# Kernel optimization log

Hardware: AMD Instinct MI355X
Metric: run time of the kernel (lower is better)

Reference implementation:

```python
import jax, jax.numpy as jnp
import numpy as np

B, S, E = 4, 2048, 1024


def setup_inputs() -> dict:
    key = jax.random.key(0)
    k1, k2, k3, k4 = jax.random.split(key, 4)
    scale = 1.0 / np.sqrt(E)
    return {
        "x": jax.random.normal(k1, (B, S, E), dtype=jnp.float32),
        "W_Q": jax.random.normal(k2, (E, E), dtype=jnp.float32) * scale,
        "W_K": jax.random.normal(k3, (E, E), dtype=jnp.float32) * scale,
        "W_V": jax.random.normal(k4, (E, E), dtype=jnp.float32) * scale,
    }


def reference(x, W_Q, W_K, W_V):
    # nn.Linear(E, E, bias=False): y = x @ W.T
    Q = jnp.einsum("bse,fe->bsf", x, W_Q)
    K = jnp.einsum("bse,fe->bsf", x, W_K)
    V = jnp.einsum("bse,fe->bsf", x, W_V)
    d = Q.shape[-1]
    scores = jnp.einsum("bqd,bkd->bqk", Q, K) / jnp.sqrt(jnp.float32(d))
    # causal mask: -inf strictly above the diagonal
    seq = Q.shape[1]
    causal = jnp.tril(jnp.ones((seq, seq), dtype=bool))  # [S,S]
    scores = jnp.where(causal[None, :, :], scores, jnp.float32(-jnp.inf))
    attn = jax.nn.softmax(scores, axis=-1)
    return jnp.einsum("bqk,bkd->bqd", attn, V)
```

## Files before the change

### kernel.cpp

```cpp
#include <hip/hip_runtime.h>
#include <hip/hip_bf16.h>
#include <stdint.h>

typedef __hip_bfloat16 bf16;
typedef __attribute__((ext_vector_type(8))) short bf16x8;
typedef __attribute__((ext_vector_type(4))) float f32x4;
typedef __attribute__((ext_vector_type(8))) unsigned short u16x8;
typedef __attribute__((ext_vector_type(4))) unsigned short u16x4;

#define SLEN 2048
#define ED   1024
#define NB   4
#define AS1 __attribute__((address_space(1)))
#define AS3 __attribute__((address_space(3)))
#define SB0() __builtin_amdgcn_sched_barrier(0)

static __device__ __forceinline__ unsigned short f2bf(float f) {
    return __builtin_bit_cast(unsigned short, __float2bfloat16(f));
}

__device__ __forceinline__ void gemm_core(
    const char* __restrict__ aT, int lda,
    const char* __restrict__ bT, int ldb,
    int nkt, char* sm, int tid, f32x4 (&acc)[4][4])
{
    const int lane = tid & 63, wave = tid >> 6;
    const int wm = wave >> 1, wn = wave & 1;
    const int fr = lane & 15, kc = lane >> 4;

    auto STAGE = [&](int kh, int Tn) {
        char* buf = sm + (Tn & 1) * 49152;
#pragma unroll
        for (int j = 0; j < 2; ++j) {
            int rid = j * 512 + tid;
            int row = rid >> 2, c = rid & 3;
            const char* src = aT + (size_t)row * lda + Tn * 128 + kh * 64
                            + ((c ^ ((row >> 1) & 3)) * 16);
            __builtin_amdgcn_global_load_lds(
                (const AS1 uint32_t*)src,
                (AS3 uint32_t*)(buf + kh * 16384 + (j * 512 + wave * 64) * 16),
                16, 0, 0);
        }
        {
            int row = tid >> 2, c = tid & 3;
            const char* src = bT + (size_t)row * ldb + Tn * 128 + kh * 64
                            + ((c ^ ((row >> 1) & 3)) * 16);
            __builtin_amdgcn_global_load_lds(
                (const AS1 uint32_t*)src,
                (AS3 uint32_t*)(buf + 32768 + kh * 8192 + (wave * 64) * 16),
                16, 0, 0);
        }
    };
    auto RD = [&](int T, int kh, bf16x8 (&a)[4], bf16x8 (&b)[4]) {
        const char* buf = sm + (T & 1) * 49152;
#pragma unroll
        for (int i = 0; i < 4; ++i) {
            int row = wm * 64 + i * 16 + fr;
            a[i] = *(const bf16x8*)(buf + kh * 16384 + row * 64
                                    + ((kc ^ ((row >> 1) & 3)) * 16));
        }
#pragma unroll
        for (int i = 0; i < 4; ++i) {
            int row = wn * 64 + i * 16 + fr;
            b[i] = *(const bf16x8*)(buf + 32768 + kh * 8192 + row * 64
                                    + ((kc ^ ((row >> 1) & 3)) * 16));
        }
    };
    auto MM = [&](bf16x8 (&a)[4], bf16x8 (&b)[4]) {
        __builtin_amdgcn_s_setprio(1);
#pragma unroll
        for (int i = 0; i < 4; ++i)
#pragma unroll
            for (int n = 0; n < 4; ++n)
                acc[i][n] = __builtin_amdgcn_mfma_f32_16x16x32_bf16(
                    a[i], b[n], acc[i][n], 0, 0, 0);
        __builtin_amdgcn_s_setprio(0);
    };

    STAGE(0, 0); STAGE(1, 0);
    asm volatile("s_waitcnt vmcnt(3)" ::: "memory");
    SB0();
    __builtin_amdgcn_s_barrier();

    bf16x8 aE[4], bE[4], aO[4], bO[4];
    for (int T = 0; T < nkt; ++T) {
        const bool pre = (T + 1 < nkt);
        RD(T, 0, aE, bE);
        SB0();
        if (pre) STAGE(0, T + 1);
        SB0();
        if (T > 0) {
            asm volatile("s_waitcnt lgkmcnt(8)" ::: "memory");
            SB0();
            MM(aO, bO);
        }
        if (pre) asm volatile("s_waitcnt vmcnt(3)" ::: "memory");
        else     asm volatile("s_waitcnt vmcnt(0)" ::: "memory");
        SB0();
        __builtin_amdgcn_s_barrier();
        RD(T, 1, aO, bO);
        SB0();
        if (pre) STAGE(1, T + 1);
        SB0();
        asm volatile("s_waitcnt lgkmcnt(8)" ::: "memory");
        SB0();
        MM(aE, bE);
        if (pre) asm volatile("s_waitcnt vmcnt(3)" ::: "memory");
        else     asm volatile("s_waitcnt vmcnt(0)" ::: "memory");
        SB0();
        __builtin_amdgcn_s_barrier();
    }
    asm volatile("s_waitcnt lgkmcnt(0)" ::: "memory");
    SB0();
    MM(aO, bO);
}

__global__ __launch_bounds__(256) void convert_to_bf16(
    const float* __restrict__ x, const float* __restrict__ wq,
    const float* __restrict__ wk, const float* __restrict__ wv,
    bf16* __restrict__ xb, bf16* __restrict__ wqb,
    bf16* __restrict__ wkb, bf16* __restrict__ wvb)
{
    long g = (long)blockIdx.x * 256 + threadIdx.x;
    const float* src; bf16* dst; long o;
    if (g < 1048576) { src = x; dst = xb; o = g * 8; }
    else {
        long g2 = g - 1048576;
        int w = (int)(g2 >> 17);
        o = (g2 & 131071) * 8;
        src = (w == 0) ? wq : (w == 1) ? wk : wv;
        dst = (w == 0) ? wqb : (w == 1) ? wkb : wvb;
    }
    float4 v0 = *(const float4*)(src + o);
    float4 v1 = *(const float4*)(src + o + 4);
    u16x8 r;
    r[0] = f2bf(v0.x); r[1] = f2bf(v0.y); r[2] = f2bf(v0.z); r[3] = f2bf(v0.w);
    r[4] = f2bf(v1.x); r[5] = f2bf(v1.y); r[6] = f2bf(v1.z); r[7] = f2bf(v1.w);
    *(u16x8*)(dst + o) = r;
}

__global__ __launch_bounds__(512, 2) void qkv_gemm(
    const bf16* __restrict__ xb, const bf16* __restrict__ wqb,
    const bf16* __restrict__ wkb, const bf16* __restrict__ wvb,
    bf16* __restrict__ Qb, bf16* __restrict__ Kb, bf16* __restrict__ Vt)
{
    extern __shared__ char smem[];
    int bid = blockIdx.x, tid = threadIdx.x;
    int xcd = bid & 7, i = bid >> 3;
    int tm = (xcd << 2) | (i & 3);
    int tn = i >> 2;
    const bf16* W = (tn < 8) ? wqb : (tn < 16) ? wkb : wvb;
    int tnl = tn & 7;
    f32x4 acc[4][4] = {};
    gemm_core((const char*)(xb + (size_t)tm * 256 * ED), ED * 2,
              (const char*)(W + (size_t)tnl * 128 * ED), ED * 2,
              16, smem, tid, acc);

    int lane = tid & 63, wave = tid >> 6, wm = wave >> 1, wn = wave & 1;
    int rl = (lane >> 4) * 4, cl = lane & 15;
    if (tn < 16) {
        bf16* C = (tn < 8) ? Qb : Kb;
#pragma unroll
        for (int mf = 0; mf < 4; ++mf)
#pragma unroll
            for (int j = 0; j < 4; ++j) {
                int r = tm * 256 + wm * 64 + mf * 16 + rl + j;
#pragma unroll
                for (int nf = 0; nf < 4; ++nf) {
                    int c = tnl * 128 + wn * 64 + nf * 16 + cl;
                    C[(size_t)r * ED + c] = __float2bfloat16(acc[mf][nf][j]);
                }
            }
    } else {
#pragma unroll
        for (int mf = 0; mf < 4; ++mf)
#pragma unroll
            for (int j = 0; j < 4; ++j) {
                int r = tm * 256 + wm * 64 + mf * 16 + rl + j;
                int bb = r >> 11, s = r & 2047;
#pragma unroll
                for (int nf = 0; nf < 4; ++nf) {
                    int d = tnl * 128 + wn * 64 + nf * 16 + cl;
                    Vt[(((size_t)bb << 10) + d) * SLEN + s] = __float2bfloat16(acc[mf][nf][j]);
                }
            }
    }
}

__global__ __launch_bounds__(512, 2) void qk_gemm(
    const bf16* __restrict__ Qb, const bf16* __restrict__ Kb, float* __restrict__ Sc)
{
    extern __shared__ char smem[];
    int bx = blockIdx.x, b = blockIdx.y, tid = threadIdx.x;
    int t = (bx & 7) * 9 + (bx >> 3);
    int ti = 0;
    while ((ti + 1) * (ti + 2) <= t) ++ti;
    int tj = t - ti * (ti + 1);
    f32x4 acc[4][4] = {};
    gemm_core((const char*)(Qb + ((size_t)b * SLEN + ti * 256) * ED), ED * 2,
              (const char*)(Kb + ((size_t)b * SLEN + tj * 128) * ED), ED * 2,
              16, smem, tid, acc);

    float* Sb = Sc + (size_t)b * SLEN * SLEN;
    int lane = tid & 63, wave = tid >> 6, wm = wave >> 1, wn = wave & 1;
    int rl = (lane >> 4) * 4, cl = lane & 15;
#pragma unroll
    for (int mf = 0; mf < 4; ++mf)
#pragma unroll
        for (int j = 0; j < 4; ++j) {
            int r = ti * 256 + wm * 64 + mf * 16 + rl + j;
#pragma unroll
            for (int nf = 0; nf < 4; ++nf) {
                int c = tj * 128 + wn * 64 + nf * 16 + cl;
                Sb[(size_t)r * SLEN + c] = acc[mf][nf][j] * 0.03125f;
            }
        }
}

__global__ __launch_bounds__(256) void softmax_rows(float* __restrict__ Sc)
{
    int q = blockIdx.x, b = blockIdx.y, tid = threadIdx.x;
    float* row = Sc + ((size_t)b * SLEN + q) * SLEN;
    int lane = tid & 63, wave = tid >> 6;
    __shared__ float red[4];

    float vals[8];
    float lmax = -3.0e38f;
#pragma unroll
    for (int r = 0; r < 2; ++r) {
        int i4 = tid + r * 256;
        if (i4 * 4 <= q) {
            float4 v = *(const float4*)(row + i4 * 4);
            vals[r * 4 + 0] = v.x; vals[r * 4 + 1] = v.y;
            vals[r * 4 + 2] = v.z; vals[r * 4 + 3] = v.w;
#pragma unroll
            for (int e = 0; e < 4; ++e) {
                int k = i4 * 4 + e;
                if (k <= q) lmax = fmaxf(lmax, vals[r * 4 + e]);
            }
        }
    }
#pragma unroll
    for (int o = 32; o > 0; o >>= 1) lmax = fmaxf(lmax, __shfl_xor(lmax, o));
    if (lane == 0) red[wave] = lmax;
    __syncthreads();
    float m = fmaxf(fmaxf(red[0], red[1]), fmaxf(red[2], red[3]));
    __syncthreads();
    float lsum = 0.f;
#pragma unroll
    for (int r = 0; r < 2; ++r) {
        int i4 = tid + r * 256;
        if (i4 * 4 <= q)
#pragma unroll
            for (int e = 0; e < 4; ++e) {
                int k = i4 * 4 + e;
                if (k <= q) lsum += __expf(vals[r * 4 + e] - m);
            }
    }
#pragma unroll
    for (int o = 32; o > 0; o >>= 1) lsum += __shfl_xor(lsum, o);
    if (lane == 0) red[wave] = lsum;
    __syncthreads();
    float inv = 1.0f / (red[0] + red[1] + red[2] + red[3]);
    unsigned short* prow = (unsigned short*)row;
#pragma unroll
    for (int r = 0; r < 2; ++r) {
        int i4 = tid + r * 256;
        u16x4 o4;
#pragma unroll
        for (int e = 0; e < 4; ++e) {
            int k = i4 * 4 + e;
            float p = (k <= q) ? __expf(vals[r * 4 + e] - m) * inv : 0.0f;
            o4[e] = f2bf(p);
        }
        *(u16x4*)(prow + i4 * 4) = o4;
    }
}

__global__ __launch_bounds__(512, 2) void pv_gemm(
    const bf16* __restrict__ P, const bf16* __restrict__ Vt, float* __restrict__ O)
{
    extern __shared__ char smem[];
    int mq = 7 - blockIdx.x, nd = blockIdx.y, b = blockIdx.z, tid = threadIdx.x;
    f32x4 acc[4][4] = {};
    int nkt = (mq + 1) * 4;
    gemm_core((const char*)P + ((size_t)b * SLEN + mq * 256) * 8192, 8192,
              (const char*)(Vt + ((size_t)b * ED + nd * 128) * SLEN), SLEN * 2,
              nkt, smem, tid, acc);

    int lane = tid & 63, wave = tid >> 6, wm = wave >> 1, wn = wave & 1;
    int rl = (lane >> 4) * 4, cl = lane & 15;
    float* Ob = O + (size_t)b * SLEN * ED;
#pragma unroll
    for (int mf = 0; mf < 4; ++mf)
#pragma unroll
        for (int j = 0; j < 4; ++j) {
            int r = mq * 256 + wm * 64 + mf * 16 + rl + j;
#pragma unroll
            for (int nf = 0; nf < 4; ++nf) {
                int c = nd * 128 + wn * 64 + nf * 16 + cl;
                Ob[(size_t)r * ED + c] = acc[mf][nf][j];
            }
        }
}

extern "C" void kernel_launch(void* const* d_in, const int* in_sizes, int n_in,
                              void* d_out, int out_size, void* d_ws, size_t ws_size,
                              hipStream_t stream)
{
    const float* x  = (const float*)d_in[0];
    const float* wq = (const float*)d_in[1];
    const float* wk = (const float*)d_in[2];
    const float* wv = (const float*)d_in[3];
    float* out = (float*)d_out;

    char* ws = (char*)d_ws;
    bf16* xb  = (bf16*)(ws);
    bf16* wqb = (bf16*)(ws + 16777216);
    bf16* wkb = (bf16*)(ws + 18874368);
    bf16* wvb = (bf16*)(ws + 20971520);
    bf16* Qb  = (bf16*)(ws + 23068672);
    bf16* Kb  = (bf16*)(ws + 39845888);
    bf16* Vt  = (bf16*)(ws + 56623104);
    float* Sc = (float*)(ws + 73400320);

    (void)hipFuncSetAttribute((const void*)qkv_gemm,
            hipFuncAttributeMaxDynamicSharedMemorySize, 98304);
    (void)hipFuncSetAttribute((const void*)qk_gemm,
            hipFuncAttributeMaxDynamicSharedMemorySize, 98304);
    (void)hipFuncSetAttribute((const void*)pv_gemm,
            hipFuncAttributeMaxDynamicSharedMemorySize, 98304);

    convert_to_bf16<<<5632, 256, 0, stream>>>(x, wq, wk, wv, xb, wqb, wkb, wvb);
    qkv_gemm<<<768, 512, 98304, stream>>>(xb, wqb, wkb, wvb, Qb, Kb, Vt);
    qk_gemm<<<dim3(72, NB), 512, 98304, stream>>>(Qb, Kb, Sc);
    softmax_rows<<<dim3(SLEN, NB), 256, 0, stream>>>(Sc);
    pv_gemm<<<dim3(8, 8, NB), 512, 98304, stream>>>((const bf16*)Sc, Vt, out);
}
```

Before: 155.1 us.

## Use 4-wave blocks with 128x64 warp tiles and 4-stage K pipeline

Rewrites the shared GEMM core to use 256-thread blocks where each wave computes a 128x64 tile with 8x4 MFMA accumulators. The k-loop now advances 64 columns per step through a four-slot LDS ring with three tiles prefetched, instead of a double buffer of 128-column tiles split into two halves. The aim is more register-level reuse of the B fragments and deeper prefetch of global memory. In exchange each wave holds many more accumulator and fragment registers and there are half as many waves per block, which lowers occupancy and latency hiding.

After: 194.1 us. +25.2%, slower.

```diff
diff --git a/kernel.cpp b/kernel.cpp
--- a/kernel.cpp
+++ b/kernel.cpp
@@ -22,97 +22,97 @@
 __device__ __forceinline__ void gemm_core(
     const char* __restrict__ aT, int lda,
     const char* __restrict__ bT, int ldb,
-    int nkt, char* sm, int tid, f32x4 (&acc)[4][4])
+    int nkt, char* sm, int tid, f32x4 (&acc)[8][4])
 {
     const int lane = tid & 63, wave = tid >> 6;
     const int wm = wave >> 1, wn = wave & 1;
     const int fr = lane & 15, kc = lane >> 4;
 
-    auto STAGE = [&](int kh, int Tn) {
-        char* buf = sm + (Tn & 1) * 49152;
-#pragma unroll
-        for (int j = 0; j < 2; ++j) {
-            int rid = j * 512 + tid;
+    auto STAGE = [&](int t) {
+        char* base = sm + (t & 3) * 24576;
+#pragma unroll
+        for (int j = 0; j < 4; ++j) {
+            int rid = j * 256 + tid;
             int row = rid >> 2, c = rid & 3;
-            const char* src = aT + (size_t)row * lda + Tn * 128 + kh * 64
+            const char* src = aT + (size_t)row * lda + t * 64
                             + ((c ^ ((row >> 1) & 3)) * 16);
             __builtin_amdgcn_global_load_lds(
                 (const AS1 uint32_t*)src,
-                (AS3 uint32_t*)(buf + kh * 16384 + (j * 512 + wave * 64) * 16),
-                16, 0, 0);
-        }
-        {
-            int row = tid >> 2, c = tid & 3;
-            const char* src = bT + (size_t)row * ldb + Tn * 128 + kh * 64
+                (AS3 uint32_t*)(base + (j * 256 + wave * 64) * 16), 16, 0, 0);
+        }
+#pragma unroll
+        for (int j = 0; j < 2; ++j) {
+            int rid = j * 256 + tid;
+            int row = rid >> 2, c = rid & 3;
+            const char* src = bT + (size_t)row * ldb + t * 64
                             + ((c ^ ((row >> 1) & 3)) * 16);
             __builtin_amdgcn_global_load_lds(
                 (const AS1 uint32_t*)src,
-                (AS3 uint32_t*)(buf + 32768 + kh * 8192 + (wave * 64) * 16),
-                16, 0, 0);
+                (AS3 uint32_t*)(base + 16384 + (j * 256 + wave * 64) * 16), 16, 0, 0);
         }
     };
-    auto RD = [&](int T, int kh, bf16x8 (&a)[4], bf16x8 (&b)[4]) {
-        const char* buf = sm + (T & 1) * 49152;
-#pragma unroll
-        for (int i = 0; i < 4; ++i) {
-            int row = wm * 64 + i * 16 + fr;
-            a[i] = *(const bf16x8*)(buf + kh * 16384 + row * 64
-                                    + ((kc ^ ((row >> 1) & 3)) * 16));
-        }
-#pragma unroll
-        for (int i = 0; i < 4; ++i) {
-            int row = wn * 64 + i * 16 + fr;
-            b[i] = *(const bf16x8*)(buf + 32768 + kh * 8192 + row * 64
-                                    + ((kc ^ ((row >> 1) & 3)) * 16));
+    auto RD = [&](int t, bf16x8 (&a)[8], bf16x8 (&b)[4]) {
+        const char* s = sm + (t & 3) * 24576;
+#pragma unroll
+        for (int i = 0; i < 8; ++i) {
+            int row = wm * 128 + i * 16 + fr;
+            a[i] = *(const bf16x8*)(s + row * 64 + ((kc ^ ((row >> 1) & 3)) * 16));
+        }
+#pragma unroll
+        for (int n = 0; n < 4; ++n) {
+            int row = wn * 64 + n * 16 + fr;
+            b[n] = *(const bf16x8*)(s + 16384 + row * 64 + ((kc ^ ((row >> 1) & 3)) * 16));
         }
     };
-    auto MM = [&](bf16x8 (&a)[4], bf16x8 (&b)[4]) {
+    auto MM = [&](bf16x8 (&a)[8], bf16x8 (&b)[4]) {
         __builtin_amdgcn_s_setprio(1);
 #pragma unroll
-        for (int i = 0; i < 4; ++i)
+        for (int i = 0; i < 8; ++i)
 #pragma unroll
             for (int n = 0; n < 4; ++n)
                 acc[i][n] = __builtin_amdgcn_mfma_f32_16x16x32_bf16(
                     a[i], b[n], acc[i][n], 0, 0, 0);
         __builtin_amdgcn_s_setprio(0);
     };
-
-    STAGE(0, 0); STAGE(1, 0);
-    asm volatile("s_waitcnt vmcnt(3)" ::: "memory");
+#define LGKM(t1ok) do { if (t1ok) asm volatile("s_waitcnt lgkmcnt(12)" ::: "memory"); \
+                        else      asm volatile("s_waitcnt lgkmcnt(0)"  ::: "memory"); } while (0)
+#define VMC(t3ok)  do { if (t3ok) asm volatile("s_waitcnt vmcnt(6)" ::: "memory"); \
+                        else      asm volatile("s_waitcnt vmcnt(0)" ::: "memory"); } while (0)
+
+    bf16x8 aE[8], bE[4], aO[8], bO[4];
+    STAGE(0); STAGE(1); STAGE(2);
+    asm volatile("s_waitcnt vmcnt(6)" ::: "memory");
     SB0();
     __builtin_amdgcn_s_barrier();
-
-    bf16x8 aE[4], bE[4], aO[4], bO[4];
-    for (int T = 0; T < nkt; ++T) {
-        const bool pre = (T + 1 < nkt);
-        RD(T, 0, aE, bE);
+    RD(0, aE, bE);
+    SB0();
+
+    for (int T = 0; T < nkt; T += 2) {
+        if (T + 1 < nkt) RD(T + 1, aO, bO);
         SB0();
-        if (pre) STAGE(0, T + 1);
+        if (T + 3 < nkt) STAGE(T + 3);
         SB0();
-        if (T > 0) {
-            asm volatile("s_waitcnt lgkmcnt(8)" ::: "memory");
+        LGKM(T + 1 < nkt);
+        SB0();
+        MM(aE, bE);
+        VMC(T + 3 < nkt);
+        SB0();
+        __builtin_amdgcn_s_barrier();
+        if (T + 1 < nkt) {
+            if (T + 2 < nkt) RD(T + 2, aE, bE);
+            SB0();
+            if (T + 4 < nkt) STAGE(T + 4);
+            SB0();
+            LGKM(T + 2 < nkt);
             SB0();
             MM(aO, bO);
-        }
-        if (pre) asm volatile("s_waitcnt vmcnt(3)" ::: "memory");
-        else     asm volatile("s_waitcnt vmcnt(0)" ::: "memory");
-        SB0();
-        __builtin_amdgcn_s_barrier();
-        RD(T, 1, aO, bO);
-        SB0();
-        if (pre) STAGE(1, T + 1);
-        SB0();
-        asm volatile("s_waitcnt lgkmcnt(8)" ::: "memory");
-        SB0();
-        MM(aE, bE);
-        if (pre) asm volatile("s_waitcnt vmcnt(3)" ::: "memory");
-        else     asm volatile("s_waitcnt vmcnt(0)" ::: "memory");
-        SB0();
-        __builtin_amdgcn_s_barrier();
-    }
-    asm volatile("s_waitcnt lgkmcnt(0)" ::: "memory");
-    SB0();
-    MM(aO, bO);
+            VMC(T + 4 < nkt);
+            SB0();
+            __builtin_amdgcn_s_barrier();
+        }
+    }
+#undef LGKM
+#undef VMC
 }
 
 __global__ __launch_bounds__(256) void convert_to_bf16(
@@ -139,7 +139,7 @@
     *(u16x8*)(dst + o) = r;
 }
 
-__global__ __launch_bounds__(512, 2) void qkv_gemm(
+__global__ __launch_bounds__(256, 1) void qkv_gemm(
     const bf16* __restrict__ xb, const bf16* __restrict__ wqb,
     const bf16* __restrict__ wkb, const bf16* __restrict__ wvb,
     bf16* __restrict__ Qb, bf16* __restrict__ Kb, bf16* __restrict__ Vt)
@@ -151,20 +151,20 @@
     int tn = i >> 2;
     const bf16* W = (tn < 8) ? wqb : (tn < 16) ? wkb : wvb;
     int tnl = tn & 7;
-    f32x4 acc[4][4] = {};
+    f32x4 acc[8][4] = {};
     gemm_core((const char*)(xb + (size_t)tm * 256 * ED), ED * 2,
               (const char*)(W + (size_t)tnl * 128 * ED), ED * 2,
-              16, smem, tid, acc);
+              32, smem, tid, acc);
 
     int lane = tid & 63, wave = tid >> 6, wm = wave >> 1, wn = wave & 1;
     int rl = (lane >> 4) * 4, cl = lane & 15;
     if (tn < 16) {
         bf16* C = (tn < 8) ? Qb : Kb;
 #pragma unroll
-        for (int mf = 0; mf < 4; ++mf)
+        for (int mf = 0; mf < 8; ++mf)
 #pragma unroll
             for (int j = 0; j < 4; ++j) {
-                int r = tm * 256 + wm * 64 + mf * 16 + rl + j;
+                int r = tm * 256 + wm * 128 + mf * 16 + rl + j;
 #pragma unroll
                 for (int nf = 0; nf < 4; ++nf) {
                     int c = tnl * 128 + wn * 64 + nf * 16 + cl;
@@ -173,10 +173,10 @@
             }
     } else {
 #pragma unroll
-        for (int mf = 0; mf < 4; ++mf)
+        for (int mf = 0; mf < 8; ++mf)
 #pragma unroll
             for (int j = 0; j < 4; ++j) {
-                int r = tm * 256 + wm * 64 + mf * 16 + rl + j;
+                int r = tm * 256 + wm * 128 + mf * 16 + rl + j;
                 int bb = r >> 11, s = r & 2047;
 #pragma unroll
                 for (int nf = 0; nf < 4; ++nf) {
@@ -187,7 +187,7 @@
     }
 }
 
-__global__ __launch_bounds__(512, 2) void qk_gemm(
+__global__ __launch_bounds__(256, 1) void qk_gemm(
     const bf16* __restrict__ Qb, const bf16* __restrict__ Kb, float* __restrict__ Sc)
 {
     extern __shared__ char smem[];
@@ -196,19 +196,19 @@
     int ti = 0;
     while ((ti + 1) * (ti + 2) <= t) ++ti;
     int tj = t - ti * (ti + 1);
-    f32x4 acc[4][4] = {};
+    f32x4 acc[8][4] = {};
     gemm_core((const char*)(Qb + ((size_t)b * SLEN + ti * 256) * ED), ED * 2,
               (const char*)(Kb + ((size_t)b * SLEN + tj * 128) * ED), ED * 2,
-              16, smem, tid, acc);
+              32, smem, tid, acc);
 
     float* Sb = Sc + (size_t)b * SLEN * SLEN;
     int lane = tid & 63, wave = tid >> 6, wm = wave >> 1, wn = wave & 1;
     int rl = (lane >> 4) * 4, cl = lane & 15;
 #pragma unroll
-    for (int mf = 0; mf < 4; ++mf)
+    for (int mf = 0; mf < 8; ++mf)
 #pragma unroll
         for (int j = 0; j < 4; ++j) {
-            int r = ti * 256 + wm * 64 + mf * 16 + rl + j;
+            int r = ti * 256 + wm * 128 + mf * 16 + rl + j;
 #pragma unroll
             for (int nf = 0; nf < 4; ++nf) {
                 int c = tj * 128 + wn * 64 + nf * 16 + cl;
@@ -277,13 +277,13 @@
     }
 }
 
-__global__ __launch_bounds__(512, 2) void pv_gemm(
+__global__ __launch_bounds__(256, 1) void pv_gemm(
     const bf16* __restrict__ P, const bf16* __restrict__ Vt, float* __restrict__ O)
 {
     extern __shared__ char smem[];
     int mq = 7 - blockIdx.x, nd = blockIdx.y, b = blockIdx.z, tid = threadIdx.x;
-    f32x4 acc[4][4] = {};
-    int nkt = (mq + 1) * 4;
+    f32x4 acc[8][4] = {};
+    int nkt = (mq + 1) * 8;
     gemm_core((const char*)P + ((size_t)b * SLEN + mq * 256) * 8192, 8192,
               (const char*)(Vt + ((size_t)b * ED + nd * 128) * SLEN), SLEN * 2,
               nkt, smem, tid, acc);
@@ -292,10 +292,10 @@
     int rl = (lane >> 4) * 4, cl = lane & 15;
     float* Ob = O + (size_t)b * SLEN * ED;
 #pragma unroll
-    for (int mf = 0; mf < 4; ++mf)
+    for (int mf = 0; mf < 8; ++mf)
 #pragma unroll
         for (int j = 0; j < 4; ++j) {
-            int r = mq * 256 + wm * 64 + mf * 16 + rl + j;
+            int r = mq * 256 + wm * 128 + mf * 16 + rl + j;
 #pragma unroll
             for (int nf = 0; nf < 4; ++nf) {
                 int c = nd * 128 + wn * 64 + nf * 16 + cl;
@@ -332,8 +332,8 @@
             hipFuncAttributeMaxDynamicSharedMemorySize, 98304);
 
     convert_to_bf16<<<5632, 256, 0, stream>>>(x, wq, wk, wv, xb, wqb, wkb, wvb);
-    qkv_gemm<<<768, 512, 98304, stream>>>(xb, wqb, wkb, wvb, Qb, Kb, Vt);
-    qk_gemm<<<dim3(72, NB), 512, 98304, stream>>>(Qb, Kb, Sc);
+    qkv_gemm<<<768, 256, 98304, stream>>>(xb, wqb, wkb, wvb, Qb, Kb, Vt);
+    qk_gemm<<<dim3(72, NB), 256, 98304, stream>>>(Qb, Kb, Sc);
     softmax_rows<<<dim3(SLEN, NB), 256, 0, stream>>>(Sc);
-    pv_gemm<<<dim3(8, 8, NB), 512, 98304, stream>>>((const bf16*)Sc, Vt, out);
-}
+    pv_gemm<<<dim3(8, 8, NB), 256, 98304, stream>>>((const bf16*)Sc, Vt, out);
+}
```

## Switch GEMM core to triple-buffered 64-wide K tiles and raise occupancy bounds

Applied to the files above, without the earlier changes.

Restructures the shared GEMM main loop from a double-buffered 128-wide K pipeline into a three-slot ring of 64-wide K stages, lowering shared memory per block from 96 KB to 72 KB. Tile counts are doubled accordingly, and the loop alternates register fragment sets across two stages per iteration with full vmcnt waits. Launch bounds are raised to request four blocks per CU, which tightens the register budget and may cause spilling of the accumulator fragments, while LDS still limits residency.

After: 456.6 us. 194% more time.

```diff
diff --git a/kernel.cpp b/kernel.cpp
--- a/kernel.cpp
+++ b/kernel.cpp
@@ -28,42 +28,38 @@
     const int wm = wave >> 1, wn = wave & 1;
     const int fr = lane & 15, kc = lane >> 4;
 
-    auto STAGE = [&](int kh, int Tn) {
-        char* buf = sm + (Tn & 1) * 49152;
+    auto STAGE = [&](int t) {
+        char* base = sm + (t % 3) * 24576;
 #pragma unroll
         for (int j = 0; j < 2; ++j) {
             int rid = j * 512 + tid;
             int row = rid >> 2, c = rid & 3;
-            const char* src = aT + (size_t)row * lda + Tn * 128 + kh * 64
+            const char* src = aT + (size_t)row * lda + t * 64
                             + ((c ^ ((row >> 1) & 3)) * 16);
             __builtin_amdgcn_global_load_lds(
                 (const AS1 uint32_t*)src,
-                (AS3 uint32_t*)(buf + kh * 16384 + (j * 512 + wave * 64) * 16),
-                16, 0, 0);
+                (AS3 uint32_t*)(base + (j * 512 + wave * 64) * 16), 16, 0, 0);
         }
         {
             int row = tid >> 2, c = tid & 3;
-            const char* src = bT + (size_t)row * ldb + Tn * 128 + kh * 64
+            const char* src = bT + (size_t)row * ldb + t * 64
                             + ((c ^ ((row >> 1) & 3)) * 16);
             __builtin_amdgcn_global_load_lds(
                 (const AS1 uint32_t*)src,
-                (AS3 uint32_t*)(buf + 32768 + kh * 8192 + (wave * 64) * 16),
-                16, 0, 0);
+                (AS3 uint32_t*)(base + 16384 + (wave * 64) * 16), 16, 0, 0);
         }
     };
-    auto RD = [&](int T, int kh, bf16x8 (&a)[4], bf16x8 (&b)[4]) {
-        const char* buf = sm + (T & 1) * 49152;
+    auto RD = [&](int t, bf16x8 (&a)[4], bf16x8 (&b)[4]) {
+        const char* s = sm + (t % 3) * 24576;
 #pragma unroll
         for (int i = 0; i < 4; ++i) {
             int row = wm * 64 + i * 16 + fr;
-            a[i] = *(const bf16x8*)(buf + kh * 16384 + row * 64
-                                    + ((kc ^ ((row >> 1) & 3)) * 16));
-        }
-#pragma unroll
-        for (int i = 0; i < 4; ++i) {
-            int row = wn * 64 + i * 16 + fr;
-            b[i] = *(const bf16x8*)(buf + 32768 + kh * 8192 + row * 64
-                                    + ((kc ^ ((row >> 1) & 3)) * 16));
+            a[i] = *(const bf16x8*)(s + row * 64 + ((kc ^ ((row >> 1) & 3)) * 16));
+        }
+#pragma unroll
+        for (int n = 0; n < 4; ++n) {
+            int row = wn * 64 + n * 16 + fr;
+            b[n] = *(const bf16x8*)(s + 16384 + row * 64 + ((kc ^ ((row >> 1) & 3)) * 16));
         }
     };
     auto MM = [&](bf16x8 (&a)[4], bf16x8 (&b)[4]) {
@@ -77,42 +73,42 @@
         __builtin_amdgcn_s_setprio(0);
     };
 
-    STAGE(0, 0); STAGE(1, 0);
-    asm volatile("s_waitcnt vmcnt(3)" ::: "memory");
+    bf16x8 aE[4], bE[4], aO[4], bO[4];
+    STAGE(0); STAGE(1);
+    asm volatile("s_waitcnt vmcnt(0)" ::: "memory");
     SB0();
     __builtin_amdgcn_s_barrier();
-
-    bf16x8 aE[4], bE[4], aO[4], bO[4];
-    for (int T = 0; T < nkt; ++T) {
-        const bool pre = (T + 1 < nkt);
-        RD(T, 0, aE, bE);
-        SB0();
-        if (pre) STAGE(0, T + 1);
-        SB0();
-        if (T > 0) {
+    RD(0, aE, bE);
+    SB0();
+
+    for (int T = 0; T < nkt; T += 2) {
+        if (T + 2 < nkt) STAGE(T + 2);
+        SB0();
+        RD(T + 1, aO, bO);
+        SB0();
+        asm volatile("s_waitcnt lgkmcnt(8)" ::: "memory");
+        SB0();
+        MM(aE, bE);
+        asm volatile("s_waitcnt vmcnt(0)" ::: "memory");
+        SB0();
+        __builtin_amdgcn_s_barrier();
+        if (T + 3 < nkt) STAGE(T + 3);
+        SB0();
+        if (T + 2 < nkt) {
+            RD(T + 2, aE, bE);
+            SB0();
             asm volatile("s_waitcnt lgkmcnt(8)" ::: "memory");
+        } else {
+            asm volatile("s_waitcnt lgkmcnt(0)" ::: "memory");
+        }
+        SB0();
+        MM(aO, bO);
+        if (T + 2 < nkt) {
+            asm volatile("s_waitcnt vmcnt(0)" ::: "memory");
             SB0();
-            MM(aO, bO);
-        }
-        if (pre) asm volatile("s_waitcnt vmcnt(3)" ::: "memory");
-        else     asm volatile("s_waitcnt vmcnt(0)" ::: "memory");
-        SB0();
-        __builtin_amdgcn_s_barrier();
-        RD(T, 1, aO, bO);
-        SB0();
-        if (pre) STAGE(1, T + 1);
-        SB0();
-        asm volatile("s_waitcnt lgkmcnt(8)" ::: "memory");
-        SB0();
-        MM(aE, bE);
-        if (pre) asm volatile("s_waitcnt vmcnt(3)" ::: "memory");
-        else     asm volatile("s_waitcnt vmcnt(0)" ::: "memory");
-        SB0();
-        __builtin_amdgcn_s_barrier();
-    }
-    asm volatile("s_waitcnt lgkmcnt(0)" ::: "memory");
-    SB0();
-    MM(aO, bO);
+            __builtin_amdgcn_s_barrier();
+        }
+    }
 }
 
 __global__ __launch_bounds__(256) void convert_to_bf16(
@@ -139,7 +135,7 @@
     *(u16x8*)(dst + o) = r;
 }
 
-__global__ __launch_bounds__(512, 2) void qkv_gemm(
+__global__ __launch_bounds__(512, 4) void qkv_gemm(
     const bf16* __restrict__ xb, const bf16* __restrict__ wqb,
     const bf16* __restrict__ wkb, const bf16* __restrict__ wvb,
     bf16* __restrict__ Qb, bf16* __restrict__ Kb, bf16* __restrict__ Vt)
@@ -154,7 +150,7 @@
     f32x4 acc[4][4] = {};
     gemm_core((const char*)(xb + (size_t)tm * 256 * ED), ED * 2,
               (const char*)(W + (size_t)tnl * 128 * ED), ED * 2,
-              16, smem, tid, acc);
+              32, smem, tid, acc);
 
     int lane = tid & 63, wave = tid >> 6, wm = wave >> 1, wn = wave & 1;
     int rl = (lane >> 4) * 4, cl = lane & 15;
@@ -187,7 +183,7 @@
     }
 }
 
-__global__ __launch_bounds__(512, 2) void qk_gemm(
+__global__ __launch_bounds__(512, 4) void qk_gemm(
     const bf16* __restrict__ Qb, const bf16* __restrict__ Kb, float* __restrict__ Sc)
 {
     extern __shared__ char smem[];
@@ -199,7 +195,7 @@
     f32x4 acc[4][4] = {};
     gemm_core((const char*)(Qb + ((size_t)b * SLEN + ti * 256) * ED), ED * 2,
               (const char*)(Kb + ((size_t)b * SLEN + tj * 128) * ED), ED * 2,
-              16, smem, tid, acc);
+              32, smem, tid, acc);
 
     float* Sb = Sc + (size_t)b * SLEN * SLEN;
     int lane = tid & 63, wave = tid >> 6, wm = wave >> 1, wn = wave & 1;
@@ -277,13 +273,13 @@
     }
 }
 
-__global__ __launch_bounds__(512, 2) void pv_gemm(
+__global__ __launch_bounds__(512, 4) void pv_gemm(
     const bf16* __restrict__ P, const bf16* __restrict__ Vt, float* __restrict__ O)
 {
     extern __shared__ char smem[];
     int mq = 7 - blockIdx.x, nd = blockIdx.y, b = blockIdx.z, tid = threadIdx.x;
     f32x4 acc[4][4] = {};
-    int nkt = (mq + 1) * 4;
+    int nkt = (mq + 1) * 8;
     gemm_core((const char*)P + ((size_t)b * SLEN + mq * 256) * 8192, 8192,
               (const char*)(Vt + ((size_t)b * ED + nd * 128) * SLEN), SLEN * 2,
               nkt, smem, tid, acc);
@@ -325,15 +321,15 @@
     float* Sc = (float*)(ws + 73400320);
 
     (void)hipFuncSetAttribute((const void*)qkv_gemm,
-            hipFuncAttributeMaxDynamicSharedMemorySize, 98304);
+            hipFuncAttributeMaxDynamicSharedMemorySize, 73728);
     (void)hipFuncSetAttribute((const void*)qk_gemm,
-            hipFuncAttributeMaxDynamicSharedMemorySize, 98304);
+            hipFuncAttributeMaxDynamicSharedMemorySize, 73728);
     (void)hipFuncSetAttribute((const void*)pv_gemm,
-            hipFuncAttributeMaxDynamicSharedMemorySize, 98304);
+            hipFuncAttributeMaxDynamicSharedMemorySize, 73728);
 
     convert_to_bf16<<<5632, 256, 0, stream>>>(x, wq, wk, wv, xb, wqb, wkb, wvb);
-    qkv_gemm<<<768, 512, 98304, stream>>>(xb, wqb, wkb, wvb, Qb, Kb, Vt);
-    qk_gemm<<<dim3(72, NB), 512, 98304, stream>>>(Qb, Kb, Sc);
+    qkv_gemm<<<768, 512, 73728, stream>>>(xb, wqb, wkb, wvb, Qb, Kb, Vt);
+    qk_gemm<<<dim3(72, NB), 512, 73728, stream>>>(Qb, Kb, Sc);
     softmax_rows<<<dim3(SLEN, NB), 256, 0, stream>>>(Sc);
-    pv_gemm<<<dim3(8, 8, NB), 512, 98304, stream>>>((const bf16*)Sc, Vt, out);
-}
+    pv_gemm<<<dim3(8, 8, NB), 512, 73728, stream>>>((const bf16*)Sc, Vt, out);
+}
```

## Split-K the long causal PV tiles with atomic accumulation and reorder block schedule

Applied to the files above, without the earlier changes.

The PV GEMM now splits the four longest row tiles (mq 4..7) into two K-halves that accumulate into the output with float atomicAdd, so the work per block is more even across the causal triangle. Blocks are scheduled heaviest-first on a flat grid of 384. A new zero_tail kernel clears the lower half of the output rows beforehand so the atomics start from zero. This trades an extra launch, atomic traffic and non-deterministic summation order for better load balance. gemm_core is renamed to gemm_core8.

Result: slower. 165.0 us (+6.4%).

```diff
diff --git a/kernel.cpp b/kernel.cpp
--- a/kernel.cpp
+++ b/kernel.cpp
@@ -19,7 +19,7 @@
     return __builtin_bit_cast(unsigned short, __float2bfloat16(f));
 }
 
-__device__ __forceinline__ void gemm_core(
+__device__ __forceinline__ void gemm_core8(
     const char* __restrict__ aT, int lda,
     const char* __restrict__ bT, int ldb,
     int nkt, char* sm, int tid, f32x4 (&acc)[4][4])
@@ -152,9 +152,9 @@
     const bf16* W = (tn < 8) ? wqb : (tn < 16) ? wkb : wvb;
     int tnl = tn & 7;
     f32x4 acc[4][4] = {};
-    gemm_core((const char*)(xb + (size_t)tm * 256 * ED), ED * 2,
-              (const char*)(W + (size_t)tnl * 128 * ED), ED * 2,
-              16, smem, tid, acc);
+    gemm_core8((const char*)(xb + (size_t)tm * 256 * ED), ED * 2,
+               (const char*)(W + (size_t)tnl * 128 * ED), ED * 2,
+               16, smem, tid, acc);
 
     int lane = tid & 63, wave = tid >> 6, wm = wave >> 1, wn = wave & 1;
     int rl = (lane >> 4) * 4, cl = lane & 15;
@@ -197,9 +197,9 @@
     while ((ti + 1) * (ti + 2) <= t) ++ti;
     int tj = t - ti * (ti + 1);
     f32x4 acc[4][4] = {};
-    gemm_core((const char*)(Qb + ((size_t)b * SLEN + ti * 256) * ED), ED * 2,
-              (const char*)(Kb + ((size_t)b * SLEN + tj * 128) * ED), ED * 2,
-              16, smem, tid, acc);
+    gemm_core8((const char*)(Qb + ((size_t)b * SLEN + ti * 256) * ED), ED * 2,
+               (const char*)(Kb + ((size_t)b * SLEN + tj * 128) * ED), ED * 2,
+               16, smem, tid, acc);
 
     float* Sb = Sc + (size_t)b * SLEN * SLEN;
     int lane = tid & 63, wave = tid >> 6, wm = wave >> 1, wn = wave & 1;
@@ -277,31 +277,64 @@
     }
 }
 
+__global__ __launch_bounds__(256) void zero_tail(float* __restrict__ O)
+{
+    int t = blockIdx.x * 256 + threadIdx.x;
+    int b = t >> 18, rem = t & 262143;
+    float4* O4 = (float4*)O;
+    O4[((size_t)b * SLEN + 1024) * (ED / 4) + rem] = make_float4(0.f, 0.f, 0.f, 0.f);
+}
+
 __global__ __launch_bounds__(512, 2) void pv_gemm(
     const bf16* __restrict__ P, const bf16* __restrict__ Vt, float* __restrict__ O)
 {
     extern __shared__ char smem[];
-    int mq = 7 - blockIdx.x, nd = blockIdx.y, b = blockIdx.z, tid = threadIdx.x;
+    int g = blockIdx.x, tid = threadIdx.x;
+    int mq, nd, b, h, isHalf;
+    if (g < 64)       { isHalf = 1; mq = 7; int w = g;       h = w & 1; b = (w >> 1) & 3; nd = (w >> 3) & 7; }
+    else if (g < 96)  { isHalf = 0; mq = 3; int w = g - 64;  h = 0;     b = w & 3;        nd = (w >> 2) & 7; }
+    else if (g < 160) { isHalf = 1; mq = 6; int w = g - 96;  h = w & 1; b = (w >> 1) & 3; nd = (w >> 3) & 7; }
+    else if (g < 224) { isHalf = 1; mq = 5; int w = g - 160; h = w & 1; b = (w >> 1) & 3; nd = (w >> 3) & 7; }
+    else if (g < 256) { isHalf = 0; mq = 2; int w = g - 224; h = 0;     b = w & 3;        nd = (w >> 2) & 7; }
+    else if (g < 320) { isHalf = 1; mq = 4; int w = g - 256; h = w & 1; b = (w >> 1) & 3; nd = (w >> 3) & 7; }
+    else if (g < 352) { isHalf = 0; mq = 1; int w = g - 320; h = 0;     b = w & 3;        nd = (w >> 2) & 7; }
+    else              { isHalf = 0; mq = 0; int w = g - 352; h = 0;     b = w & 3;        nd = (w >> 2) & 7; }
+
+    int nkt = isHalf ? (mq + 1) * 2 : (mq + 1) * 4;
+    size_t koff = (size_t)h * (mq + 1) * 128 * 2;
     f32x4 acc[4][4] = {};
-    int nkt = (mq + 1) * 4;
-    gemm_core((const char*)P + ((size_t)b * SLEN + mq * 256) * 8192, 8192,
-              (const char*)(Vt + ((size_t)b * ED + nd * 128) * SLEN), SLEN * 2,
-              nkt, smem, tid, acc);
+    gemm_core8((const char*)P + ((size_t)b * SLEN + mq * 256) * 8192 + koff, 8192,
+               (const char*)(Vt + ((size_t)b * ED + nd * 128) * SLEN) + koff, SLEN * 2,
+               nkt, smem, tid, acc);
 
     int lane = tid & 63, wave = tid >> 6, wm = wave >> 1, wn = wave & 1;
     int rl = (lane >> 4) * 4, cl = lane & 15;
     float* Ob = O + (size_t)b * SLEN * ED;
-#pragma unroll
-    for (int mf = 0; mf < 4; ++mf)
-#pragma unroll
-        for (int j = 0; j < 4; ++j) {
-            int r = mq * 256 + wm * 64 + mf * 16 + rl + j;
-#pragma unroll
-            for (int nf = 0; nf < 4; ++nf) {
-                int c = nd * 128 + wn * 64 + nf * 16 + cl;
-                Ob[(size_t)r * ED + c] = acc[mf][nf][j];
-            }
-        }
+    if (isHalf) {
+#pragma unroll
+        for (int mf = 0; mf < 4; ++mf)
+#pragma unroll
+            for (int j = 0; j < 4; ++j) {
+                int r = mq * 256 + wm * 64 + mf * 16 + rl + j;
+#pragma unroll
+                for (int nf = 0; nf < 4; ++nf) {
+                    int c = nd * 128 + wn * 64 + nf * 16 + cl;
+                    atomicAdd(&Ob[(size_t)r * ED + c], acc[mf][nf][j]);
+                }
+            }
+    } else {
+#pragma unroll
+        for (int mf = 0; mf < 4; ++mf)
+#pragma unroll
+            for (int j = 0; j < 4; ++j) {
+                int r = mq * 256 + wm * 64 + mf * 16 + rl + j;
+#pragma unroll
+                for (int nf = 0; nf < 4; ++nf) {
+                    int c = nd * 128 + wn * 64 + nf * 16 + cl;
+                    Ob[(size_t)r * ED + c] = acc[mf][nf][j];
+                }
+            }
+    }
 }
 
 extern "C" void kernel_launch(void* const* d_in, const int* in_sizes, int n_in,
@@ -335,5 +368,6 @@
     qkv_gemm<<<768, 512, 98304, stream>>>(xb, wqb, wkb, wvb, Qb, Kb, Vt);
     qk_gemm<<<dim3(72, NB), 512, 98304, stream>>>(Qb, Kb, Sc);
     softmax_rows<<<dim3(SLEN, NB), 256, 0, stream>>>(Sc);
-    pv_gemm<<<dim3(8, 8, NB), 512, 98304, stream>>>((const bf16*)Sc, Vt, out);
-}
+    zero_tail<<<4096, 256, 0, stream>>>(out);
+    pv_gemm<<<384, 512, 98304, stream>>>((const bf16*)Sc, Vt, out);
+}
```
